# Kernel optimization log

Hardware: AMD Instinct MI355X
Metric: run time of the kernel (lower is better)

## Reference

```python
import jax, jax.numpy as jnp
import numpy as np

N_NODES = 40000
FEAT = 128
HID = 128
EMB = 64
N_EDGES = 640000


def setup_inputs() -> dict:
    key = jax.random.key(0)
    ks = jax.random.split(key, 8)
    x = jax.random.normal(ks[0], (N_NODES, FEAT), dtype=jnp.float32)
    edge_index = jax.random.randint(ks[1], (2, N_EDGES), 0, N_NODES, dtype=jnp.int64)
    s1 = 1.0 / np.sqrt(FEAT)
    s2 = 1.0 / np.sqrt(HID)
    W1_l = jax.random.uniform(ks[2], (HID, FEAT), jnp.float32, -s1, s1)
    b1 = jax.random.uniform(ks[3], (HID,), jnp.float32, -s1, s1)
    W1_r = jax.random.uniform(ks[4], (HID, FEAT), jnp.float32, -s1, s1)
    W2_l = jax.random.uniform(ks[5], (EMB, HID), jnp.float32, -s2, s2)
    b2 = jax.random.uniform(ks[6], (EMB,), jnp.float32, -s2, s2)
    W2_r = jax.random.uniform(ks[7], (EMB, HID), jnp.float32, -s2, s2)
    return {"x": x, "edge_index": edge_index, "W1_l": W1_l, "b1": b1,
            "W1_r": W1_r, "W2_l": W2_l, "b2": b2, "W2_r": W2_r}


def _sage_conv(x, src, dst, W_l, b_l, W_r, n_nodes):
    # mean aggregation of source-node features onto destination nodes
    msg = x[src]                                           # [E, d]
    agg = jax.ops.segment_sum(msg, dst, num_segments=n_nodes)   # [N, d]
    cnt = jax.ops.segment_sum(jnp.ones((src.shape[0],), x.dtype), dst,
                              num_segments=n_nodes)        # [N]
    agg = agg / jnp.maximum(cnt, 1.0)[:, None]
    # out = lin_l(mean_j x_j) + lin_r(x_i); bias lives in lin_l
    return agg @ W_l.T + b_l + x @ W_r.T


def reference(x, edge_index, W1_l, b1, W1_r, W2_l, b2, W2_r):
    src, dst = edge_index[0], edge_index[1]
    n = x.shape[0]
    h = _sage_conv(x, src, dst, W1_l, b1, W1_r, n)
    h = jax.nn.elu(h)
    # dropout p=0.2 is identity in eval mode
    h = _sage_conv(h, src, dst, W2_l, b2, W2_r, n)
    return jax.nn.log_softmax(h, axis=1)
```

## Files before the change

kernel.cpp:

```cpp
#include <hip/hip_runtime.h>
#include <hip/hip_fp16.h>
#include <math.h>

#define N_NODES 40000
#define FEATD 128
#define EMB 64
#define N_EDGES 640000
#define CAP 64

typedef unsigned short u16;
typedef __attribute__((ext_vector_type(8))) short s16x8;
typedef __attribute__((ext_vector_type(8))) unsigned short u16x8;
typedef __attribute__((ext_vector_type(4))) float f32x4;

__device__ __forceinline__ u16 f2bf(float f) {
  unsigned u = __float_as_uint(f);
  u += 0x7FFF + ((u >> 16) & 1);
  return (u16)(u >> 16);
}
__device__ __forceinline__ float bf2f(u16 h) {
  return __uint_as_float(((unsigned)h) << 16);
}
__device__ __forceinline__ float h2f(u16 h) {
  __half hh;
  *(u16*)&hh = h;
  return __half2float(hh);
}
__device__ __forceinline__ u16 f2h(float f) {
  __half hh = __float2half(f);
  return *(u16*)&hh;
}

__global__ __launch_bounds__(256) void prep_weights(
    const float* __restrict__ W1l, const float* __restrict__ W1r,
    const float* __restrict__ W2l, const float* __restrict__ W2r,
    u16* __restrict__ wp) {
  int i = blockIdx.x * 256 + threadIdx.x;
  const float* srcp;
  u16* hi;
  int off;
  if (i < 16384)       { srcp = W1l; off = i;          hi = wp; }
  else if (i < 32768)  { srcp = W1r; off = i - 16384;  hi = wp + 32768; }
  else if (i < 40960)  { srcp = W2l; off = i - 32768;  hi = wp + 65536; }
  else                 { srcp = W2r; off = i - 40960;  hi = wp + 81920; }
  float v = srcp[off];
  u16 h = f2bf(v);
  hi[off] = h;
  hi[off + ((i < 32768) ? 16384 : 8192)] = f2bf(v - bf2f(h));
}

__global__ __launch_bounds__(256) void convert_x(
    const float* __restrict__ x, u16* __restrict__ xh) {
  int i = blockIdx.x * 256 + threadIdx.x;
  float4 v0 = *(const float4*)(&x[i * 8]);
  float4 v1 = *(const float4*)(&x[i * 8 + 4]);
  u16x8 o;
  o[0] = f2h(v0.x); o[1] = f2h(v0.y); o[2] = f2h(v0.z); o[3] = f2h(v0.w);
  o[4] = f2h(v1.x); o[5] = f2h(v1.y); o[6] = f2h(v1.z); o[7] = f2h(v1.w);
  *(u16x8*)(&xh[i * 8]) = o;
}

__global__ __launch_bounds__(256) void fill_kernel(
    const int* __restrict__ src, const int* __restrict__ dst,
    int* __restrict__ deg, u16* __restrict__ bucket) {
  int e = blockIdx.x * 256 + threadIdx.x;
  if (e >= N_EDGES) return;
  int s = src[e];
  int d = dst[e];
  int pos = atomicAdd(&deg[d], 1);
  if (pos < CAP) bucket[d * CAP + pos] = (u16)s;
}

__global__ __launch_bounds__(256) void gather_mean_f16(
    const u16* __restrict__ xh, const int* __restrict__ deg,
    const u16* __restrict__ bucket, u16* __restrict__ aggh) {
  int n = blockIdx.x * 4 + (threadIdx.x >> 6);
  int lane = threadIdx.x & 63;
  int g = lane >> 4;
  int li = lane & 15;
  int dgf = deg[n];
  int dg = dgf < CAP ? dgf : CAP;
  float inv = 1.0f / fmaxf((float)dgf, 1.0f);
  const u16* bk = bucket + n * CAP;
  float acc[8];
#pragma unroll
  for (int i = 0; i < 8; i++) acc[i] = 0.f;
  for (int d = g; d < dg; d += 4) {
    u16x8 v = *(const u16x8*)(&xh[(int)bk[d] * 128 + li * 8]);
#pragma unroll
    for (int i = 0; i < 8; i++) acc[i] += h2f(v[i]);
  }
#pragma unroll
  for (int i = 0; i < 8; i++) {
    acc[i] += __shfl_xor(acc[i], 16);
    acc[i] += __shfl_xor(acc[i], 32);
  }
  if (g == 0) {
    u16x8 o;
#pragma unroll
    for (int i = 0; i < 8; i++) o[i] = f2h(acc[i] * inv);
    *(u16x8*)(&aggh[n * 128 + li * 8]) = o;
  }
}

__global__ __launch_bounds__(256) void gemm12_kernel(
    const u16* __restrict__ AggH, const u16* __restrict__ XH,
    const u16* __restrict__ wp, const float* __restrict__ b1v,
    const float* __restrict__ b2v, u16* __restrict__ Yh,
    float* __restrict__ Z) {
  const u16* w1l_hi = wp;
  const u16* w1l_lo = wp + 16384;
  const u16* w1r_hi = wp + 32768;
  const u16* w1r_lo = wp + 49152;
  const u16* w2l_hi = wp + 65536;
  const u16* w2l_lo = wp + 73728;
  const u16* w2r_hi = wp + 81920;
  const u16* w2r_lo = wp + 90112;

  __shared__ __align__(16) union {
    struct {
      u16 wl_hi[128][32], wl_lo[128][32];
      u16 wr_hi[128][32], wr_lo[128][32];
      u16 a_hi[64][32], a_lo[64][32];
      u16 x_hi[64][32], x_lo[64][32];
    } p1;
    struct {
      u16 h_hi[64][136], h_lo[64][136];
      u16 w2l_hi[64][32], w2l_lo[64][32];
      u16 w2r_hi[64][32], w2r_lo[64][32];
    } p2;
  } L;

  const int tid = threadIdx.x;
  const int wv = tid >> 6;
  const int lane = tid & 63;
  const int li = lane & 15;
  const int q = lane >> 4;
  const int nbase = blockIdx.x * 64;

  f32x4 acc1[8];
#pragma unroll
  for (int jt = 0; jt < 8; jt++) acc1[jt] = (f32x4){0.f, 0.f, 0.f, 0.f};

  for (int kb = 0; kb < 4; kb++) {
#pragma unroll
    for (int it = 0; it < 2; it++) {
      int idx = tid + 256 * it;
      int j = idx >> 2, c = idx & 3;
      int go = j * 128 + kb * 32 + c * 8;
      *(u16x8*)(&L.p1.wl_hi[j][c * 8]) = *(const u16x8*)(&w1l_hi[go]);
      *(u16x8*)(&L.p1.wl_lo[j][c * 8]) = *(const u16x8*)(&w1l_lo[go]);
      *(u16x8*)(&L.p1.wr_hi[j][c * 8]) = *(const u16x8*)(&w1r_hi[go]);
      *(u16x8*)(&L.p1.wr_lo[j][c * 8]) = *(const u16x8*)(&w1r_lo[go]);
    }
    {
      int n = tid >> 2, c = tid & 3;
      int go = (nbase + n) * 128 + kb * 32 + c * 8;
      u16x8 va = *(const u16x8*)(&AggH[go]);
      u16x8 vx = *(const u16x8*)(&XH[go]);
      u16x8 ah, al, xhv, xl;
#pragma unroll
      for (int i = 0; i < 8; i++) {
        float fa = h2f(va[i]);
        float fx = h2f(vx[i]);
        ah[i] = f2bf(fa); al[i] = f2bf(fa - bf2f(ah[i]));
        xhv[i] = f2bf(fx); xl[i] = f2bf(fx - bf2f(xhv[i]));
      }
      *(u16x8*)(&L.p1.a_hi[n][c * 8]) = ah;
      *(u16x8*)(&L.p1.a_lo[n][c * 8]) = al;
      *(u16x8*)(&L.p1.x_hi[n][c * 8]) = xhv;
      *(u16x8*)(&L.p1.x_lo[n][c * 8]) = xl;
    }
    __syncthreads();
    s16x8 aHi = *(const s16x8*)(&L.p1.a_hi[wv * 16 + li][q * 8]);
    s16x8 aLo = *(const s16x8*)(&L.p1.a_lo[wv * 16 + li][q * 8]);
    s16x8 xHi = *(const s16x8*)(&L.p1.x_hi[wv * 16 + li][q * 8]);
    s16x8 xLo = *(const s16x8*)(&L.p1.x_lo[wv * 16 + li][q * 8]);
#pragma unroll
    for (int jt = 0; jt < 8; jt++) {
      s16x8 wlHi = *(const s16x8*)(&L.p1.wl_hi[jt * 16 + li][q * 8]);
      s16x8 wlLo = *(const s16x8*)(&L.p1.wl_lo[jt * 16 + li][q * 8]);
      s16x8 wrHi = *(const s16x8*)(&L.p1.wr_hi[jt * 16 + li][q * 8]);
      s16x8 wrLo = *(const s16x8*)(&L.p1.wr_lo[jt * 16 + li][q * 8]);
      f32x4 a = acc1[jt];
      a = __builtin_amdgcn_mfma_f32_16x16x32_bf16(aHi, wlHi, a, 0, 0, 0);
      a = __builtin_amdgcn_mfma_f32_16x16x32_bf16(aLo, wlHi, a, 0, 0, 0);
      a = __builtin_amdgcn_mfma_f32_16x16x32_bf16(aHi, wlLo, a, 0, 0, 0);
      a = __builtin_amdgcn_mfma_f32_16x16x32_bf16(xHi, wrHi, a, 0, 0, 0);
      a = __builtin_amdgcn_mfma_f32_16x16x32_bf16(xLo, wrHi, a, 0, 0, 0);
      a = __builtin_amdgcn_mfma_f32_16x16x32_bf16(xHi, wrLo, a, 0, 0, 0);
      acc1[jt] = a;
    }
    __syncthreads();
  }

#pragma unroll
  for (int jt = 0; jt < 8; jt++) {
    int j = jt * 16 + li;
    float bb = b1v[j];
#pragma unroll
    for (int r = 0; r < 4; r++) {
      float v = acc1[jt][r] + bb;
      v = v > 0.f ? v : expm1f(v);
      int nl = wv * 16 + q * 4 + r;
      u16 hi = f2bf(v);
      L.p2.h_hi[nl][j] = hi;
      L.p2.h_lo[nl][j] = f2bf(v - bf2f(hi));
    }
  }

  f32x4 accY[4], accZ[4];
#pragma unroll
  for (int mt = 0; mt < 4; mt++) {
    accY[mt] = (f32x4){0.f, 0.f, 0.f, 0.f};
    accZ[mt] = (f32x4){0.f, 0.f, 0.f, 0.f};
  }
  for (int kb = 0; kb < 4; kb++) {
    {
      int j = tid >> 2, c = tid & 3;
      int go = j * 128 + kb * 32 + c * 8;
      *(u16x8*)(&L.p2.w2l_hi[j][c * 8]) = *(const u16x8*)(&w2l_hi[go]);
      *(u16x8*)(&L.p2.w2l_lo[j][c * 8]) = *(const u16x8*)(&w2l_lo[go]);
      *(u16x8*)(&L.p2.w2r_hi[j][c * 8]) = *(const u16x8*)(&w2r_hi[go]);
      *(u16x8*)(&L.p2.w2r_lo[j][c * 8]) = *(const u16x8*)(&w2r_lo[go]);
    }
    __syncthreads();
    s16x8 blHi = *(const s16x8*)(&L.p2.w2l_hi[wv * 16 + li][q * 8]);
    s16x8 blLo = *(const s16x8*)(&L.p2.w2l_lo[wv * 16 + li][q * 8]);
    s16x8 brHi = *(const s16x8*)(&L.p2.w2r_hi[wv * 16 + li][q * 8]);
    s16x8 brLo = *(const s16x8*)(&L.p2.w2r_lo[wv * 16 + li][q * 8]);
#pragma unroll
    for (int mt = 0; mt < 4; mt++) {
      s16x8 hHi = *(const s16x8*)(&L.p2.h_hi[mt * 16 + li][kb * 32 + q * 8]);
      s16x8 hLo = *(const s16x8*)(&L.p2.h_lo[mt * 16 + li][kb * 32 + q * 8]);
      f32x4 ay = accY[mt];
      ay = __builtin_amdgcn_mfma_f32_16x16x32_bf16(hHi, blHi, ay, 0, 0, 0);
      ay = __builtin_amdgcn_mfma_f32_16x16x32_bf16(hLo, blHi, ay, 0, 0, 0);
      ay = __builtin_amdgcn_mfma_f32_16x16x32_bf16(hHi, blLo, ay, 0, 0, 0);
      accY[mt] = ay;
      f32x4 az = accZ[mt];
      az = __builtin_amdgcn_mfma_f32_16x16x32_bf16(hHi, brHi, az, 0, 0, 0);
      az = __builtin_amdgcn_mfma_f32_16x16x32_bf16(hLo, brHi, az, 0, 0, 0);
      az = __builtin_amdgcn_mfma_f32_16x16x32_bf16(hHi, brLo, az, 0, 0, 0);
      accZ[mt] = az;
    }
    __syncthreads();
  }

  {
    int j2 = wv * 16 + li;
    float bb = b2v[j2];
#pragma unroll
    for (int mt = 0; mt < 4; mt++) {
#pragma unroll
      for (int r = 0; r < 4; r++) {
        int node = nbase + mt * 16 + q * 4 + r;
        Yh[node * 64 + j2] = f2h(accY[mt][r]);
        Z[node * 64 + j2] = accZ[mt][r] + bb;
      }
    }
  }
}

__global__ __launch_bounds__(256) void final_kernel(
    const u16* __restrict__ Y, const float* __restrict__ Z,
    const int* __restrict__ deg, const u16* __restrict__ bucket,
    float* __restrict__ out) {
  int n = blockIdx.x * 4 + (threadIdx.x >> 6);
  int lane = threadIdx.x & 63;
  int g = lane >> 4;
  int li = lane & 15;
  int dgf = deg[n];
  int dg = dgf < CAP ? dgf : CAP;
  float inv = 1.0f / fmaxf((float)dgf, 1.0f);
  const u16* bk = bucket + n * CAP;
  float4 acc = {0.f, 0.f, 0.f, 0.f};
  for (int d = g; d < dg; d += 4) {
    ushort4 v = *(const ushort4*)(&Y[(int)bk[d] * 64 + li * 4]);
    acc.x += h2f(v.x); acc.y += h2f(v.y); acc.z += h2f(v.z); acc.w += h2f(v.w);
  }
  acc.x += __shfl_xor(acc.x, 16); acc.y += __shfl_xor(acc.y, 16);
  acc.z += __shfl_xor(acc.z, 16); acc.w += __shfl_xor(acc.w, 16);
  acc.x += __shfl_xor(acc.x, 32); acc.y += __shfl_xor(acc.y, 32);
  acc.z += __shfl_xor(acc.z, 32); acc.w += __shfl_xor(acc.w, 32);
  float4 zb = *(const float4*)(&Z[n * 64 + li * 4]);
  float4 v;
  v.x = zb.x + acc.x * inv; v.y = zb.y + acc.y * inv;
  v.z = zb.z + acc.z * inv; v.w = zb.w + acc.w * inv;
  float m = fmaxf(fmaxf(v.x, v.y), fmaxf(v.z, v.w));
  m = fmaxf(m, __shfl_xor(m, 1)); m = fmaxf(m, __shfl_xor(m, 2));
  m = fmaxf(m, __shfl_xor(m, 4)); m = fmaxf(m, __shfl_xor(m, 8));
  float s = __expf(v.x - m) + __expf(v.y - m) + __expf(v.z - m) + __expf(v.w - m);
  s += __shfl_xor(s, 1); s += __shfl_xor(s, 2);
  s += __shfl_xor(s, 4); s += __shfl_xor(s, 8);
  float lg = m + logf(s);
  if (lane < 16) {
    float4 o = {v.x - lg, v.y - lg, v.z - lg, v.w - lg};
    *(float4*)(&out[n * 64 + li * 4]) = o;
  }
}

extern "C" void kernel_launch(void* const* d_in, const int* in_sizes, int n_in,
                              void* d_out, int out_size, void* d_ws, size_t ws_size,
                              hipStream_t stream) {
  const float* x   = (const float*)d_in[0];
  const int*   ei  = (const int*)d_in[1];
  const float* W1l = (const float*)d_in[2];
  const float* b1  = (const float*)d_in[3];
  const float* W1r = (const float*)d_in[4];
  const float* W2l = (const float*)d_in[5];
  const float* b2  = (const float*)d_in[6];
  const float* W2r = (const float*)d_in[7];
  float* out = (float*)d_out;

  const int* src = ei;
  const int* dst = ei + N_EDGES;

  u16* bucket = (u16*)d_ws;
  int* deg = (int*)(bucket + (size_t)N_NODES * CAP);
  u16* xh = (u16*)(deg + N_NODES);
  u16* aggh = xh + (size_t)N_NODES * FEATD;
  u16* yh = aggh + (size_t)N_NODES * FEATD;
  float* z = (float*)(yh + (size_t)N_NODES * EMB);
  u16* wp = (u16*)(z + (size_t)N_NODES * EMB);

  hipMemsetAsync(deg, 0, N_NODES * sizeof(int), stream);
  prep_weights<<<192, 256, 0, stream>>>(W1l, W1r, W2l, W2r, wp);
  convert_x<<<2500, 256, 0, stream>>>(x, xh);
  fill_kernel<<<(N_EDGES + 255) / 256, 256, 0, stream>>>(src, dst, deg, bucket);

  gather_mean_f16<<<N_NODES / 4, 256, 0, stream>>>(xh, deg, bucket, aggh);
  gemm12_kernel<<<N_NODES / 64, 256, 0, stream>>>(aggh, xh, wp, b1, b2, yh, z);
  final_kernel<<<N_NODES / 4, 256, 0, stream>>>(yh, z, deg, bucket, out);
}
```

Baseline: 202.2 us.

## Replace split-bf16 triple MFMA with single fp16 MFMA and merge prep kernels

Drops the hi/lo bf16 split emulation of fp32 in the fused GEMM kernel and uses fp16 MFMA directly on the fp16 activations and fp16-converted weights, cutting MFMA count and LDS traffic roughly threefold. The K-loop is restructured into fewer, larger tiles with padded LDS rows, and layer-2 weights are loaded once rather than per K-block. The weight and x conversion kernels are merged into one launch. The cost is lower precision (fp16 weights and hidden activations without a residual term), which could affect accuracy tolerance.

```diff
diff --git a/kernel.cpp b/kernel.cpp
--- a/kernel.cpp
+++ b/kernel.cpp
@@ -9,18 +9,10 @@
 #define CAP 64
 
 typedef unsigned short u16;
-typedef __attribute__((ext_vector_type(8))) short s16x8;
 typedef __attribute__((ext_vector_type(8))) unsigned short u16x8;
+typedef __attribute__((ext_vector_type(8))) _Float16 f16x8;
 typedef __attribute__((ext_vector_type(4))) float f32x4;
 
-__device__ __forceinline__ u16 f2bf(float f) {
-  unsigned u = __float_as_uint(f);
-  u += 0x7FFF + ((u >> 16) & 1);
-  return (u16)(u >> 16);
-}
-__device__ __forceinline__ float bf2f(u16 h) {
-  return __uint_as_float(((unsigned)h) << 16);
-}
 __device__ __forceinline__ float h2f(u16 h) {
   __half hh;
   *(u16*)&hh = h;
@@ -31,33 +23,30 @@
   return *(u16*)&hh;
 }
 
-__global__ __launch_bounds__(256) void prep_weights(
-    const float* __restrict__ W1l, const float* __restrict__ W1r,
-    const float* __restrict__ W2l, const float* __restrict__ W2r,
+__global__ __launch_bounds__(256) void prep_kernel(
+    const float* __restrict__ x, const float* __restrict__ W1l,
+    const float* __restrict__ W1r, const float* __restrict__ W2l,
+    const float* __restrict__ W2r, u16* __restrict__ xh,
     u16* __restrict__ wp) {
-  int i = blockIdx.x * 256 + threadIdx.x;
-  const float* srcp;
-  u16* hi;
-  int off;
-  if (i < 16384)       { srcp = W1l; off = i;          hi = wp; }
-  else if (i < 32768)  { srcp = W1r; off = i - 16384;  hi = wp + 32768; }
-  else if (i < 40960)  { srcp = W2l; off = i - 32768;  hi = wp + 65536; }
-  else                 { srcp = W2r; off = i - 40960;  hi = wp + 81920; }
-  float v = srcp[off];
-  u16 h = f2bf(v);
-  hi[off] = h;
-  hi[off + ((i < 32768) ? 16384 : 8192)] = f2bf(v - bf2f(h));
-}
-
-__global__ __launch_bounds__(256) void convert_x(
-    const float* __restrict__ x, u16* __restrict__ xh) {
-  int i = blockIdx.x * 256 + threadIdx.x;
-  float4 v0 = *(const float4*)(&x[i * 8]);
-  float4 v1 = *(const float4*)(&x[i * 8 + 4]);
-  u16x8 o;
-  o[0] = f2h(v0.x); o[1] = f2h(v0.y); o[2] = f2h(v0.z); o[3] = f2h(v0.w);
-  o[4] = f2h(v1.x); o[5] = f2h(v1.y); o[6] = f2h(v1.z); o[7] = f2h(v1.w);
-  *(u16x8*)(&xh[i * 8]) = o;
+  int bid = blockIdx.x;
+  if (bid < 2500) {
+    int i = bid * 256 + threadIdx.x;
+    float4 v0 = *(const float4*)(&x[i * 8]);
+    float4 v1 = *(const float4*)(&x[i * 8 + 4]);
+    u16x8 o;
+    o[0] = f2h(v0.x); o[1] = f2h(v0.y); o[2] = f2h(v0.z); o[3] = f2h(v0.w);
+    o[4] = f2h(v1.x); o[5] = f2h(v1.y); o[6] = f2h(v1.z); o[7] = f2h(v1.w);
+    *(u16x8*)(&xh[i * 8]) = o;
+  } else {
+    int i = (bid - 2500) * 256 + threadIdx.x;
+    const float* srcp;
+    int off;
+    if (i < 16384)      { srcp = W1l; off = i; }
+    else if (i < 32768) { srcp = W1r; off = i - 16384; }
+    else if (i < 40960) { srcp = W2l; off = i - 32768; }
+    else                { srcp = W2r; off = i - 40960; }
+    wp[i] = f2h(srcp[off]);
+  }
 }
 
 __global__ __launch_bounds__(256) void fill_kernel(
@@ -108,26 +97,19 @@
     const u16* __restrict__ wp, const float* __restrict__ b1v,
     const float* __restrict__ b2v, u16* __restrict__ Yh,
     float* __restrict__ Z) {
-  const u16* w1l_hi = wp;
-  const u16* w1l_lo = wp + 16384;
-  const u16* w1r_hi = wp + 32768;
-  const u16* w1r_lo = wp + 49152;
-  const u16* w2l_hi = wp + 65536;
-  const u16* w2l_lo = wp + 73728;
-  const u16* w2r_hi = wp + 81920;
-  const u16* w2r_lo = wp + 90112;
+  const u16* w1l = wp;
+  const u16* w1r = wp + 16384;
+  const u16* w2l = wp + 32768;
+  const u16* w2r = wp + 40960;
 
   __shared__ __align__(16) union {
     struct {
-      u16 wl_hi[128][32], wl_lo[128][32];
-      u16 wr_hi[128][32], wr_lo[128][32];
-      u16 a_hi[64][32], a_lo[64][32];
-      u16 x_hi[64][32], x_lo[64][32];
+      u16 wl[128][72], wr[128][72];
+      u16 a[64][72], x[64][72];
     } p1;
     struct {
-      u16 h_hi[64][136], h_lo[64][136];
-      u16 w2l_hi[64][32], w2l_lo[64][32];
-      u16 w2r_hi[64][32], w2r_lo[64][32];
+      u16 h[64][136];
+      u16 w2l[64][136], w2r[64][136];
     } p2;
   } L;
 
@@ -142,54 +124,35 @@
 #pragma unroll
   for (int jt = 0; jt < 8; jt++) acc1[jt] = (f32x4){0.f, 0.f, 0.f, 0.f};
 
-  for (int kb = 0; kb < 4; kb++) {
+  for (int kb = 0; kb < 2; kb++) {
+#pragma unroll
+    for (int it = 0; it < 4; it++) {
+      int idx = tid + 256 * it;
+      int j = idx >> 3, c = idx & 7;
+      int go = j * 128 + kb * 64 + c * 8;
+      *(u16x8*)(&L.p1.wl[j][c * 8]) = *(const u16x8*)(&w1l[go]);
+      *(u16x8*)(&L.p1.wr[j][c * 8]) = *(const u16x8*)(&w1r[go]);
+    }
 #pragma unroll
     for (int it = 0; it < 2; it++) {
       int idx = tid + 256 * it;
-      int j = idx >> 2, c = idx & 3;
-      int go = j * 128 + kb * 32 + c * 8;
-      *(u16x8*)(&L.p1.wl_hi[j][c * 8]) = *(const u16x8*)(&w1l_hi[go]);
-      *(u16x8*)(&L.p1.wl_lo[j][c * 8]) = *(const u16x8*)(&w1l_lo[go]);
-      *(u16x8*)(&L.p1.wr_hi[j][c * 8]) = *(const u16x8*)(&w1r_hi[go]);
-      *(u16x8*)(&L.p1.wr_lo[j][c * 8]) = *(const u16x8*)(&w1r_lo[go]);
-    }
-    {
-      int n = tid >> 2, c = tid & 3;
-      int go = (nbase + n) * 128 + kb * 32 + c * 8;
-      u16x8 va = *(const u16x8*)(&AggH[go]);
-      u16x8 vx = *(const u16x8*)(&XH[go]);
-      u16x8 ah, al, xhv, xl;
-#pragma unroll
-      for (int i = 0; i < 8; i++) {
-        float fa = h2f(va[i]);
-        float fx = h2f(vx[i]);
-        ah[i] = f2bf(fa); al[i] = f2bf(fa - bf2f(ah[i]));
-        xhv[i] = f2bf(fx); xl[i] = f2bf(fx - bf2f(xhv[i]));
+      int n = idx >> 3, c = idx & 7;
+      int go = (nbase + n) * 128 + kb * 64 + c * 8;
+      *(u16x8*)(&L.p1.a[n][c * 8]) = *(const u16x8*)(&AggH[go]);
+      *(u16x8*)(&L.p1.x[n][c * 8]) = *(const u16x8*)(&XH[go]);
+    }
+    __syncthreads();
+#pragma unroll
+    for (int kk = 0; kk < 2; kk++) {
+      f16x8 aF = *(const f16x8*)(&L.p1.a[wv * 16 + li][kk * 32 + q * 8]);
+      f16x8 xF = *(const f16x8*)(&L.p1.x[wv * 16 + li][kk * 32 + q * 8]);
+#pragma unroll
+      for (int jt = 0; jt < 8; jt++) {
+        f16x8 wlF = *(const f16x8*)(&L.p1.wl[jt * 16 + li][kk * 32 + q * 8]);
+        f16x8 wrF = *(const f16x8*)(&L.p1.wr[jt * 16 + li][kk * 32 + q * 8]);
+        acc1[jt] = __builtin_amdgcn_mfma_f32_16x16x32_f16(aF, wlF, acc1[jt], 0, 0, 0);
+        acc1[jt] = __builtin_amdgcn_mfma_f32_16x16x32_f16(xF, wrF, acc1[jt], 0, 0, 0);
       }
-      *(u16x8*)(&L.p1.a_hi[n][c * 8]) = ah;
-      *(u16x8*)(&L.p1.a_lo[n][c * 8]) = al;
-      *(u16x8*)(&L.p1.x_hi[n][c * 8]) = xhv;
-      *(u16x8*)(&L.p1.x_lo[n][c * 8]) = xl;
-    }
-    __syncthreads();
-    s16x8 aHi = *(const s16x8*)(&L.p1.a_hi[wv * 16 + li][q * 8]);
-    s16x8 aLo = *(const s16x8*)(&L.p1.a_lo[wv * 16 + li][q * 8]);
-    s16x8 xHi = *(const s16x8*)(&L.p1.x_hi[wv * 16 + li][q * 8]);
-    s16x8 xLo = *(const s16x8*)(&L.p1.x_lo[wv * 16 + li][q * 8]);
-#pragma unroll
-    for (int jt = 0; jt < 8; jt++) {
-      s16x8 wlHi = *(const s16x8*)(&L.p1.wl_hi[jt * 16 + li][q * 8]);
-      s16x8 wlLo = *(const s16x8*)(&L.p1.wl_lo[jt * 16 + li][q * 8]);
-      s16x8 wrHi = *(const s16x8*)(&L.p1.wr_hi[jt * 16 + li][q * 8]);
-      s16x8 wrLo = *(const s16x8*)(&L.p1.wr_lo[jt * 16 + li][q * 8]);
-      f32x4 a = acc1[jt];
-      a = __builtin_amdgcn_mfma_f32_16x16x32_bf16(aHi, wlHi, a, 0, 0, 0);
-      a = __builtin_amdgcn_mfma_f32_16x16x32_bf16(aLo, wlHi, a, 0, 0, 0);
-      a = __builtin_amdgcn_mfma_f32_16x16x32_bf16(aHi, wlLo, a, 0, 0, 0);
-      a = __builtin_amdgcn_mfma_f32_16x16x32_bf16(xHi, wrHi, a, 0, 0, 0);
-      a = __builtin_amdgcn_mfma_f32_16x16x32_bf16(xLo, wrHi, a, 0, 0, 0);
-      a = __builtin_amdgcn_mfma_f32_16x16x32_bf16(xHi, wrLo, a, 0, 0, 0);
-      acc1[jt] = a;
     }
     __syncthreads();
   }
@@ -202,12 +165,18 @@
     for (int r = 0; r < 4; r++) {
       float v = acc1[jt][r] + bb;
       v = v > 0.f ? v : expm1f(v);
-      int nl = wv * 16 + q * 4 + r;
-      u16 hi = f2bf(v);
-      L.p2.h_hi[nl][j] = hi;
-      L.p2.h_lo[nl][j] = f2bf(v - bf2f(hi));
-    }
-  }
+      L.p2.h[wv * 16 + q * 4 + r][j] = f2h(v);
+    }
+  }
+#pragma unroll
+  for (int it = 0; it < 4; it++) {
+    int idx = tid + 256 * it;
+    int j = idx >> 4, c = idx & 15;
+    int go = j * 128 + c * 8;
+    *(u16x8*)(&L.p2.w2l[j][c * 8]) = *(const u16x8*)(&w2l[go]);
+    *(u16x8*)(&L.p2.w2r[j][c * 8]) = *(const u16x8*)(&w2r[go]);
+  }
+  __syncthreads();
 
   f32x4 accY[4], accZ[4];
 #pragma unroll
@@ -215,36 +184,16 @@
     accY[mt] = (f32x4){0.f, 0.f, 0.f, 0.f};
     accZ[mt] = (f32x4){0.f, 0.f, 0.f, 0.f};
   }
-  for (int kb = 0; kb < 4; kb++) {
-    {
-      int j = tid >> 2, c = tid & 3;
-      int go = j * 128 + kb * 32 + c * 8;
-      *(u16x8*)(&L.p2.w2l_hi[j][c * 8]) = *(const u16x8*)(&w2l_hi[go]);
-      *(u16x8*)(&L.p2.w2l_lo[j][c * 8]) = *(const u16x8*)(&w2l_lo[go]);
-      *(u16x8*)(&L.p2.w2r_hi[j][c * 8]) = *(const u16x8*)(&w2r_hi[go]);
-      *(u16x8*)(&L.p2.w2r_lo[j][c * 8]) = *(const u16x8*)(&w2r_lo[go]);
-    }
-    __syncthreads();
-    s16x8 blHi = *(const s16x8*)(&L.p2.w2l_hi[wv * 16 + li][q * 8]);
-    s16x8 blLo = *(const s16x8*)(&L.p2.w2l_lo[wv * 16 + li][q * 8]);
-    s16x8 brHi = *(const s16x8*)(&L.p2.w2r_hi[wv * 16 + li][q * 8]);
-    s16x8 brLo = *(const s16x8*)(&L.p2.w2r_lo[wv * 16 + li][q * 8]);
+#pragma unroll
+  for (int kc = 0; kc < 4; kc++) {
+    f16x8 blF = *(const f16x8*)(&L.p2.w2l[wv * 16 + li][kc * 32 + q * 8]);
+    f16x8 brF = *(const f16x8*)(&L.p2.w2r[wv * 16 + li][kc * 32 + q * 8]);
 #pragma unroll
     for (int mt = 0; mt < 4; mt++) {
-      s16x8 hHi = *(const s16x8*)(&L.p2.h_hi[mt * 16 + li][kb * 32 + q * 8]);
-      s16x8 hLo = *(const s16x8*)(&L.p2.h_lo[mt * 16 + li][kb * 32 + q * 8]);
-      f32x4 ay = accY[mt];
-      ay = __builtin_amdgcn_mfma_f32_16x16x32_bf16(hHi, blHi, ay, 0, 0, 0);
-      ay = __builtin_amdgcn_mfma_f32_16x16x32_bf16(hLo, blHi, ay, 0, 0, 0);
-      ay = __builtin_amdgcn_mfma_f32_16x16x32_bf16(hHi, blLo, ay, 0, 0, 0);
-      accY[mt] = ay;
-      f32x4 az = accZ[mt];
-      az = __builtin_amdgcn_mfma_f32_16x16x32_bf16(hHi, brHi, az, 0, 0, 0);
-      az = __builtin_amdgcn_mfma_f32_16x16x32_bf16(hLo, brHi, az, 0, 0, 0);
-      az = __builtin_amdgcn_mfma_f32_16x16x32_bf16(hHi, brLo, az, 0, 0, 0);
-      accZ[mt] = az;
-    }
-    __syncthreads();
+      f16x8 hF = *(const f16x8*)(&L.p2.h[mt * 16 + li][kc * 32 + q * 8]);
+      accY[mt] = __builtin_amdgcn_mfma_f32_16x16x32_f16(hF, blF, accY[mt], 0, 0, 0);
+      accZ[mt] = __builtin_amdgcn_mfma_f32_16x16x32_f16(hF, brF, accZ[mt], 0, 0, 0);
+    }
   }
 
   {
@@ -325,8 +274,7 @@
   u16* wp = (u16*)(z + (size_t)N_NODES * EMB);
 
   hipMemsetAsync(deg, 0, N_NODES * sizeof(int), stream);
-  prep_weights<<<192, 256, 0, stream>>>(W1l, W1r, W2l, W2r, wp);
-  convert_x<<<2500, 256, 0, stream>>>(x, xh);
+  prep_kernel<<<2500 + 192, 256, 0, stream>>>(x, W1l, W1r, W2l, W2r, xh, wp);
   fill_kernel<<<(N_EDGES + 255) / 256, 256, 0, stream>>>(src, dst, deg, bucket);
 
   gather_mean_f16<<<N_NODES / 4, 256, 0, stream>>>(xh, deg, bucket, aggh);
```

New measurement: 193.8 us. 1.04x faster.
